# Optimization experiments

Measured on AMD Instinct MI355X. Metric: run time of the kernel, lower is better.

## Reference

```python
import jax, jax.numpy as jnp
import numpy as np

# ---- constants from init_kwargs ----
ANCHORS = np.array([[[10., 13.], [16., 30.], [33., 23.]],
                    [[30., 61.], [62., 45.], [59., 119.]],
                    [[116., 90.], [156., 198.], [373., 326.]]], dtype=np.float32)
GRID_SIZES = [64, 128, 256]
INP_DIM = 2048
NC = 80          # num_classes (also the channel stride used by the original code)
LAMB = 1.0


def setup_inputs() -> dict:
    key = jax.random.key(0)
    ks = jax.random.split(key, 11)
    x0 = jax.random.normal(ks[0], (1, 255, 64, 64), jnp.float32)
    x1 = jax.random.normal(ks[1], (1, 255, 128, 128), jnp.float32)
    x2 = jax.random.normal(ks[2], (1, 255, 256, 256), jnp.float32)
    label_cls = jax.random.randint(ks[3], (3,), 0, 80)
    # boxes as (x0, y0, x1, y1) with strictly positive width/height (log target)
    xy0 = jax.random.uniform(ks[4], (3, 2), minval=0.0, maxval=1500.0)
    wh = jax.random.uniform(ks[5], (3, 2), minval=20.0, maxval=300.0)
    label_bbx = jnp.concatenate([xy0, xy0 + wh], axis=-1).astype(jnp.float32)
    pos_anc = jax.random.randint(ks[6], (3,), 0, 3)
    pos_x = jax.random.randint(ks[7], (3,), 0, 64)
    pos_y = jax.random.randint(ks[8], (3,), 0, 64)
    neg0 = jax.random.randint(ks[9], (64 * 64 * 3,), 0, 2).astype(jnp.int32)
    neg1 = jax.random.randint(ks[10], (128 * 128 * 3,), 0, 2).astype(jnp.int32)
    neg2 = jax.random.randint(jax.random.fold_in(key, 99), (256 * 256 * 3,), 0, 2).astype(jnp.int32)
    return {"x0": x0, "x1": x1, "x2": x2,
            "label_cls": label_cls, "label_bbx": label_bbx,
            "pos_anc": pos_anc, "pos_x": pos_x, "pos_y": pos_y,
            "neg0": neg0, "neg1": neg1, "neg2": neg2,
            "scale0": 0, "scale1": 1, "scale2": 2}


def _neg_loss(xj, negj, gs):
    # negatives are all flat indices i with negj[i] falsy, decoded exactly like the
    # original comprehension: a = i%3, row = i//(gs*3), col = (i%(gs*3))//3
    idx = jnp.arange(gs * gs * 3)
    a = idx % 3
    row = idx // (gs * 3)
    col = (idx % (gs * 3)) // 3
    y = xj[0, a * NC + 4, row, col]              # objectness logits at all cells
    mask = (negj == 0).astype(y.dtype)
    # BCEWithLogits(y, 0) = softplus(y); mean over selected (negative) cells
    return jnp.sum(jax.nn.softplus(y) * mask) / jnp.sum(mask)


def reference(x0, x1, x2, label_cls, label_bbx, pos_anc, pos_x, pos_y,
              neg0, neg1, neg2, scale0, scale1, scale2):
    xs = [x0, x1, x2]
    negs = [neg0, neg1, neg2]
    scales = [scale0, scale1, scale2]  # static python ints: pyramid level per box
    anchors = jnp.asarray(ANCHORS)
    loss_obj = jnp.float32(0.0)
    for j in range(3):  # per-scale negative objectness loss (fully vectorized gather)
        loss_obj = loss_obj + _neg_loss(xs[j], negs[j], GRID_SIZES[j])
    loss_bbx = jnp.float32(0.0)
    for j in range(3):  # loop over the few positive boxes, as the original does
        i = scales[j]
        stride = float(INP_DIM // GRID_SIZES[j])  # NB: original indexes by box idx j
        anc = anchors[j, i]                       # NB: faithful to anchors[j][i]
        col = xs[i][0, :, pos_y[j], pos_x[j]]     # [255] channel column at the cell
        a80 = pos_anc[j] * NC
        y_obj = jax.lax.dynamic_slice(col, (a80 + 4,), (1,))[0]
        loss_obj = loss_obj + jax.nn.softplus(-y_obj)                  # BCE(y, 1)
        y_cls = jax.lax.dynamic_slice(col, (a80 + 5,), (NC,))
        t_cls = jax.nn.one_hot(label_cls[j], NC, dtype=y_cls.dtype)
        loss_obj = loss_obj + jnp.mean(jax.nn.softplus(y_cls) - t_cls * y_cls)
        y_bbx = jax.lax.dynamic_slice(col, (a80,), (4,))
        b = label_bbx[j]
        x_c = (b[0] + b[2]) * 0.5
        y_c = (b[1] + b[3]) * 0.5
        w = b[2] - b[0]
        h = b[3] - b[1]
        fx = pos_x[j].astype(b.dtype)
        fy = pos_y[j].astype(b.dtype)
        t_bbx = jnp.stack([(x_c - fx * stride) / anc[0],
                           (y_c - fy * stride) / anc[1],
                           jnp.log(w / anc[0]),
                           jnp.log(h / anc[1])])
        d = jnp.abs(y_bbx - t_bbx)
        loss_bbx = loss_bbx + jnp.mean(jnp.where(d < 1.0, 0.5 * d * d, d - 0.5))
    return loss_obj + LAMB * loss_bbx
```

## Files before the change

### kernel.cpp

```cpp
#include <hip/hip_runtime.h>
#include <hip/hip_bf16.h>


#define NC 80

__device__ __forceinline__ float softplus_f(float x) {
    return fmaxf(x, 0.0f) + log1pf(__expf(-fabsf(x)));
}

__global__ __launch_bounds__(256) void yolo_neg_partials(
    const float* __restrict__ x0, const float* __restrict__ x1,
    const float* __restrict__ x2,
    const int* __restrict__ n0, const int* __restrict__ n1,
    const int* __restrict__ n2,
    float* __restrict__ ws )
{
    const int b = blockIdx.x;
    const int t = threadIdx.x;

    const float* __restrict__ x;
    const int* __restrict__ neg;
    int gs, cell;
    if (b < 16)      { x = x0; neg = n0; gs = 64;  cell = b * 256 + t; }
    else if (b < 80) { x = x1; neg = n1; gs = 128; cell = (b - 16) * 256 + t; }
    else             { x = x2; neg = n2; gs = 256; cell = (b - 80) * 256 + t; }
    const int gs2 = gs * gs;

    float num = 0.0f, den = 0.0f;
#pragma unroll
    for (int a = 0; a < 3; ++a) {
        float y = x[(4 + NC * a) * gs2 + cell];
        float m = (neg[cell * 3 + a] == 0) ? 1.0f : 0.0f;
        num += softplus_f(y) * m;
        den += m;
    }

#pragma unroll
    for (int off = 32; off > 0; off >>= 1) {
        num += __shfl_down(num, off);
        den += __shfl_down(den, off);
    }
    __shared__ float s[8];
    const int wave = t >> 6;
    if ((t & 63) == 0) { s[wave * 2] = num; s[wave * 2 + 1] = den; }
    __syncthreads();
    if (t == 0) {
        ws[b * 2]     = s[0] + s[2] + s[4] + s[6];
        ws[b * 2 + 1] = s[1] + s[3] + s[5] + s[7];
    }
}

__global__ __launch_bounds__(256) void yolo_finalize(
    const float* __restrict__ x0, const float* __restrict__ x1,
    const float* __restrict__ x2,
    const int* __restrict__ label_cls, const float* __restrict__ label_bbx,
    const int* __restrict__ pos_anc, const int* __restrict__ pos_x,
    const int* __restrict__ pos_y,
    const int* __restrict__ sc0, const int* __restrict__ sc1,
    const int* __restrict__ sc2,
    const float* __restrict__ ws, float* __restrict__ out)
{
    __shared__ float s_num[3], s_den[3], s_total;
    const int t = threadIdx.x;
    if (t < 3) { s_num[t] = 0.0f; s_den[t] = 0.0f; }
    if (t == 3) s_total = 0.0f;
    __syncthreads();

    for (int p = t; p < 336; p += 256) {
        int sc = (p < 16) ? 0 : ((p < 80) ? 1 : 2);
        atomicAdd(&s_num[sc], ws[p * 2]);
        atomicAdd(&s_den[sc], ws[p * 2 + 1]);
    }
    __syncthreads();

    float contrib;
    if (t < 255) {
        const int j = t / 85;
        const int c = t % 85;
        const int scl[3] = { sc0[0], sc1[0], sc2[0] };
        const int i = scl[j];
        const float* __restrict__ x = (i == 0) ? x0 : ((i == 1) ? x1 : x2);
        const int gs  = 64 << i;
        const int gs2 = gs * gs;
        const int a80 = pos_anc[j] * NC;
        const int cell = pos_y[j] * gs + pos_x[j];
        const float v = x[(a80 + c) * gs2 + cell];

        if (c == 4) {
            contrib = softplus_f(-v);
        } else if (c >= 5) {
            float tv = ((c - 5) == label_cls[j]) ? v : 0.0f;
            contrib = (softplus_f(v) - tv) * (1.0f / 80.0f);
        } else {
            const float ANC[3][3][2] = {
                {{10.f, 13.f}, {16.f, 30.f}, {33.f, 23.f}},
                {{30.f, 61.f}, {62.f, 45.f}, {59.f, 119.f}},
                {{116.f, 90.f}, {156.f, 198.f}, {373.f, 326.f}}};
            const float a0 = ANC[j][i][0], a1 = ANC[j][i][1];
            const float b0 = label_bbx[4 * j], b1 = label_bbx[4 * j + 1];
            const float b2 = label_bbx[4 * j + 2], b3 = label_bbx[4 * j + 3];
            const float strd = (float)(2048 / (64 << j));
            float tt;
            if (c == 0)      tt = ((b0 + b2) * 0.5f - (float)pos_x[j] * strd) / a0;
            else if (c == 1) tt = ((b1 + b3) * 0.5f - (float)pos_y[j] * strd) / a1;
            else if (c == 2) tt = logf((b2 - b0) / a0);
            else             tt = logf((b3 - b1) / a1);
            const float d = fabsf(v - tt);
            contrib = ((d < 1.0f) ? 0.5f * d * d : d - 0.5f) * 0.25f;
        }
    } else {
        contrib = s_num[0] / s_den[0] + s_num[1] / s_den[1] + s_num[2] / s_den[2];
    }

    atomicAdd(&s_total, contrib);
    __syncthreads();
    if (t == 0) out[0] = s_total;
}

extern "C" void kernel_launch(void* const* d_in, const int* in_sizes, int n_in,
                              void* d_out, int out_size, void* d_ws, size_t ws_size,
                              hipStream_t stream) {
    const float* x0 = (const float*)d_in[0];
    const float* x1 = (const float*)d_in[1];
    const float* x2 = (const float*)d_in[2];
    const int*   label_cls = (const int*)d_in[3];
    const float* label_bbx = (const float*)d_in[4];
    const int*   pos_anc = (const int*)d_in[5];
    const int*   pos_x   = (const int*)d_in[6];
    const int*   pos_y   = (const int*)d_in[7];
    const int*   n0 = (const int*)d_in[8];
    const int*   n1 = (const int*)d_in[9];
    const int*   n2 = (const int*)d_in[10];
    const int*   sc0 = (const int*)d_in[11];
    const int*   sc1 = (const int*)d_in[12];
    const int*   sc2 = (const int*)d_in[13];

    float* ws  = (float*)d_ws;
    float* out = (float*)d_out;

    yolo_neg_partials<<<336, 256, 0, stream>>>(x0, x1, x2, n0, n1, n2, ws);
    yolo_finalize<<<1, 256, 0, stream>>>(x0, x1, x2, label_cls, label_bbx,
                                         pos_anc, pos_x, pos_y,
                                         sc0, sc1, sc2, ws, out);
}
```

Before: 127.3 us.

## Fuse negative-partials and finalize kernels with flag-based inter-block handoff

Merges the two launches into one grid of producer blocks plus one consumer block. Producers publish their partial sums with release-store flags, and the consumer spins on acquire loads before reducing. The positive-cell loss is computed while waiting. This removes a second kernel launch and the serialization between the two kernels. The flags are never reset between calls, so later calls can read stale partials. Correctness also relies on all blocks being co-resident to avoid a spin deadlock.

```diff
diff --git a/kernel.cpp b/kernel.cpp
--- a/kernel.cpp
+++ b/kernel.cpp
@@ -3,77 +3,71 @@
 
 
 #define NC 80
+#define NPROD 336
+#define FLAG_MAGIC 0x5A5A5A5Au
 
 __device__ __forceinline__ float softplus_f(float x) {
     return fmaxf(x, 0.0f) + log1pf(__expf(-fabsf(x)));
 }
 
-__global__ __launch_bounds__(256) void yolo_neg_partials(
-    const float* __restrict__ x0, const float* __restrict__ x1,
-    const float* __restrict__ x2,
-    const int* __restrict__ n0, const int* __restrict__ n1,
-    const int* __restrict__ n2,
-    float* __restrict__ ws )
-{
-    const int b = blockIdx.x;
-    const int t = threadIdx.x;
-
-    const float* __restrict__ x;
-    const int* __restrict__ neg;
-    int gs, cell;
-    if (b < 16)      { x = x0; neg = n0; gs = 64;  cell = b * 256 + t; }
-    else if (b < 80) { x = x1; neg = n1; gs = 128; cell = (b - 16) * 256 + t; }
-    else             { x = x2; neg = n2; gs = 256; cell = (b - 80) * 256 + t; }
-    const int gs2 = gs * gs;
-
-    float num = 0.0f, den = 0.0f;
-#pragma unroll
-    for (int a = 0; a < 3; ++a) {
-        float y = x[(4 + NC * a) * gs2 + cell];
-        float m = (neg[cell * 3 + a] == 0) ? 1.0f : 0.0f;
-        num += softplus_f(y) * m;
-        den += m;
-    }
-
-#pragma unroll
-    for (int off = 32; off > 0; off >>= 1) {
-        num += __shfl_down(num, off);
-        den += __shfl_down(den, off);
-    }
-    __shared__ float s[8];
-    const int wave = t >> 6;
-    if ((t & 63) == 0) { s[wave * 2] = num; s[wave * 2 + 1] = den; }
-    __syncthreads();
-    if (t == 0) {
-        ws[b * 2]     = s[0] + s[2] + s[4] + s[6];
-        ws[b * 2 + 1] = s[1] + s[3] + s[5] + s[7];
-    }
-}
-
-__global__ __launch_bounds__(256) void yolo_finalize(
+__global__ __launch_bounds__(256) void yolo_fused(
     const float* __restrict__ x0, const float* __restrict__ x1,
     const float* __restrict__ x2,
     const int* __restrict__ label_cls, const float* __restrict__ label_bbx,
     const int* __restrict__ pos_anc, const int* __restrict__ pos_x,
     const int* __restrict__ pos_y,
+    const int* __restrict__ n0, const int* __restrict__ n1,
+    const int* __restrict__ n2,
     const int* __restrict__ sc0, const int* __restrict__ sc1,
     const int* __restrict__ sc2,
-    const float* __restrict__ ws, float* __restrict__ out)
+    float* __restrict__ ws,
+    unsigned* __restrict__ flags,
+    float* __restrict__ out)
 {
+    const int b = blockIdx.x;
+    const int t = threadIdx.x;
+
+    if (b < NPROD) {
+        const float* __restrict__ x;
+        const int* __restrict__ neg;
+        int gs, cell;
+        if (b < 16)      { x = x0; neg = n0; gs = 64;  cell = b * 256 + t; }
+        else if (b < 80) { x = x1; neg = n1; gs = 128; cell = (b - 16) * 256 + t; }
+        else             { x = x2; neg = n2; gs = 256; cell = (b - 80) * 256 + t; }
+        const int gs2 = gs * gs;
+
+        float num = 0.0f, den = 0.0f;
+#pragma unroll
+        for (int a = 0; a < 3; ++a) {
+            float y = x[(4 + NC * a) * gs2 + cell];
+            float m = (neg[cell * 3 + a] == 0) ? 1.0f : 0.0f;
+            num += softplus_f(y) * m;
+            den += m;
+        }
+#pragma unroll
+        for (int off = 32; off > 0; off >>= 1) {
+            num += __shfl_down(num, off);
+            den += __shfl_down(den, off);
+        }
+        __shared__ float s[8];
+        const int wave = t >> 6;
+        if ((t & 63) == 0) { s[wave * 2] = num; s[wave * 2 + 1] = den; }
+        __syncthreads();
+        if (t == 0) {
+            float nt = s[0] + s[2] + s[4] + s[6];
+            float dt = s[1] + s[3] + s[5] + s[7];
+            __hip_atomic_store(&ws[b * 2],     nt, __ATOMIC_RELAXED, __HIP_MEMORY_SCOPE_AGENT);
+            __hip_atomic_store(&ws[b * 2 + 1], dt, __ATOMIC_RELAXED, __HIP_MEMORY_SCOPE_AGENT);
+            __hip_atomic_store(&flags[b], FLAG_MAGIC, __ATOMIC_RELEASE, __HIP_MEMORY_SCOPE_AGENT);
+        }
+        return;
+    }
+
     __shared__ float s_num[3], s_den[3], s_total;
-    const int t = threadIdx.x;
     if (t < 3) { s_num[t] = 0.0f; s_den[t] = 0.0f; }
     if (t == 3) s_total = 0.0f;
-    __syncthreads();
 
-    for (int p = t; p < 336; p += 256) {
-        int sc = (p < 16) ? 0 : ((p < 80) ? 1 : 2);
-        atomicAdd(&s_num[sc], ws[p * 2]);
-        atomicAdd(&s_den[sc], ws[p * 2 + 1]);
-    }
-    __syncthreads();
-
-    float contrib;
+    float contrib = 0.0f;
     if (t < 255) {
         const int j = t / 85;
         const int c = t % 85;
@@ -108,9 +102,22 @@
             const float d = fabsf(v - tt);
             contrib = ((d < 1.0f) ? 0.5f * d * d : d - 0.5f) * 0.25f;
         }
-    } else {
+    }
+    __syncthreads();
+
+    for (int p = t; p < NPROD; p += 256) {
+        while (__hip_atomic_load(&flags[p], __ATOMIC_ACQUIRE, __HIP_MEMORY_SCOPE_AGENT)
+               != FLAG_MAGIC) {  }
+        float nu = __hip_atomic_load(&ws[p * 2],     __ATOMIC_RELAXED, __HIP_MEMORY_SCOPE_AGENT);
+        float de = __hip_atomic_load(&ws[p * 2 + 1], __ATOMIC_RELAXED, __HIP_MEMORY_SCOPE_AGENT);
+        const int sc = (p < 16) ? 0 : ((p < 80) ? 1 : 2);
+        atomicAdd(&s_num[sc], nu);
+        atomicAdd(&s_den[sc], de);
+    }
+    __syncthreads();
+
+    if (t == 255)
         contrib = s_num[0] / s_den[0] + s_num[1] / s_den[1] + s_num[2] / s_den[2];
-    }
 
     atomicAdd(&s_total, contrib);
     __syncthreads();
@@ -135,11 +142,11 @@
     const int*   sc1 = (const int*)d_in[12];
     const int*   sc2 = (const int*)d_in[13];
 
-    float* ws  = (float*)d_ws;
-    float* out = (float*)d_out;
+    float*    ws    = (float*)d_ws;
+    unsigned* flags = (unsigned*)(ws + 2 * NPROD);
+    float*    out   = (float*)d_out;
 
-    yolo_neg_partials<<<336, 256, 0, stream>>>(x0, x1, x2, n0, n1, n2, ws);
-    yolo_finalize<<<1, 256, 0, stream>>>(x0, x1, x2, label_cls, label_bbx,
-                                         pos_anc, pos_x, pos_y,
-                                         sc0, sc1, sc2, ws, out);
+    yolo_fused<<<NPROD + 1, 256, 0, stream>>>(
+        x0, x1, x2, label_cls, label_bbx, pos_anc, pos_x, pos_y,
+        n0, n1, n2, sc0, sc1, sc2, ws, flags, out);
 }
```

Result: no change. 127.1 us (-0.1%).
